# Kernel tuning notes

Measured on AMD Instinct MI355X. Metric: run time of the kernel, lower is better.

Reference implementation:

```python
import jax, jax.numpy as jnp
import numpy as np

G, N, H = 64, 512, 64          # graphs, nodes/graph, hidden
NT = G * N                     # total nodes
DEG = 32
ET = NT * DEG                  # total edges
KP = int(np.ceil(0.7 * N))     # TopKPooling keep per graph (359)
NP2 = G * KP                   # nodes after pooling
F_IN, NC, NA = 128, 2, 6
seg = jax.ops.segment_sum


def graph_norm(h, batch, num_g, w, b, ms, eps=1e-5):
    cnt = seg(jnp.ones((h.shape[0], 1), h.dtype), batch, num_segments=num_g)
    mean = seg(h, batch, num_segments=num_g) / cnt
    hc = h - ms * mean[batch]
    var = seg(hc * hc, batch, num_segments=num_g) / cnt
    return w * hc / jnp.sqrt(var[batch] + eps) + b


def sage(h, src, tgt, valid, Ws, Wn, b, n_nodes):
    # PyG SAGEConv (mean aggr): out_i = x_i@Ws + mean_{j->i} x_j @ Wn + b
    msg = h[src] * valid[:, None]
    agg = seg(msg, tgt, num_segments=n_nodes)
    deg = seg(valid, tgt, num_segments=n_nodes)
    return h @ Ws + (agg / jnp.maximum(deg, 1.0)[:, None]) @ Wn + b


def setup_inputs() -> dict:
    key = jax.random.key(0)
    ks = jax.random.split(key, 20)
    offs = (jnp.arange(G) * N)[:, None]
    src = (jax.random.randint(ks[0], (G, N * DEG), 0, N) + offs).reshape(-1)
    tgt = (jax.random.randint(ks[1], (G, N * DEG), 0, N) + offs).reshape(-1)
    edge_index = jnp.stack([src, tgt])  # within-graph edges

    def lin(k, fi, fo):
        return jax.random.normal(k, (fi, fo), jnp.float32) / np.sqrt(fi)

    return {
        "x": jax.random.normal(ks[2], (NT, F_IN), jnp.float32),
        "edge_index": edge_index,
        "edge_attr": jax.random.uniform(ks[3], (ET,), jnp.float32),
        "coords": jax.random.normal(ks[4], (NT, 3), jnp.float32),
        "anatomical_class": jax.random.randint(ks[5], (NT,), 0, NA),
        "Bk_table": jax.random.normal(ks[6], (NA, H * H), jnp.float32) * 0.05,
        "pos_W": lin(ks[7], 3, H), "pos_b": jnp.zeros((H,), jnp.float32),
        "W1_self": lin(ks[8], F_IN, H), "W1_neigh": lin(ks[9], F_IN, H),
        "b1": jnp.zeros((H,), jnp.float32),
        "gn1_w": jnp.ones((H,), jnp.float32), "gn1_b": jnp.zeros((H,), jnp.float32),
        "gn1_ms": jnp.ones((H,), jnp.float32),
        "pool_p": jax.random.normal(ks[10], (H,), jnp.float32),
        "W2_self": lin(ks[11], H, H), "W2_neigh": lin(ks[12], H, H),
        "b2": jnp.zeros((H,), jnp.float32),
        "gn2_w": jnp.ones((H,), jnp.float32), "gn2_b": jnp.zeros((H,), jnp.float32),
        "gn2_ms": jnp.ones((H,), jnp.float32),
        "lin1_W": lin(ks[13], 3 * H, H), "lin1_b": jnp.zeros((H,), jnp.float32),
        "lin2_W": lin(ks[14], H, NC), "lin2_b": jnp.zeros((NC,), jnp.float32),
    }


def reference(x, edge_index, edge_attr, coords, anatomical_class, Bk_table,
              pos_W, pos_b, W1_self, W1_neigh, b1, gn1_w, gn1_b, gn1_ms,
              pool_p, W2_self, W2_neigh, b2, gn2_w, gn2_b, gn2_ms,
              lin1_W, lin1_b, lin2_W, lin2_b):
    row, col = edge_index[0], edge_index[1]
    batch = jnp.repeat(jnp.arange(G), N)
    # ---- stage 1: anatomical propagation kernel ----
    e = coords @ pos_W + pos_b                                 # [NT, H]
    Ae = seg(edge_attr[:, None] * e[col], row, num_segments=NT)  # SpMM adj @ e
    Bk = Bk_table[anatomical_class].reshape(NT, H, H)
    delta = jnp.einsum('nd,nhd->nh', Ae, Bk)                   # bmm(Ae, Bk^T)
    ones_e = jnp.ones((ET,), x.dtype)
    h = sage(x, row, col, ones_e, W1_self, W1_neigh, b1, NT)
    h = jax.nn.elu(graph_norm(h, batch, G, gn1_w, gn1_b, gn1_ms))
    h = h + delta
    h = jnp.einsum('nij,nj->ni', Bk + delta[:, :, None], h)    # propagate_message
    # ---- TopK pooling (equal-sized graphs) ----
    score = (h @ pool_p) / jnp.linalg.norm(pool_p)
    vals, idx = jax.lax.top_k(score.reshape(G, N), KP)
    perm = (idx + (jnp.arange(G) * N)[:, None]).reshape(-1)    # [NP2]
    h = h[perm] * jnp.tanh(vals).reshape(-1)[:, None]
    batch2 = jnp.repeat(jnp.arange(G), KP)
    node_map = jnp.full((NT,), -1, jnp.int32).at[perm].set(jnp.arange(NP2, dtype=jnp.int32))
    s2, t2 = node_map[row], node_map[col]
    valid = ((s2 >= 0) & (t2 >= 0)).astype(h.dtype)            # masked edge filter
    s2 = jnp.where(s2 >= 0, s2, 0)
    t2 = jnp.where(t2 >= 0, t2, 0)
    # ---- stage 2 ----
    e2 = coords[perm] @ pos_W + pos_b
    Bk2 = Bk_table[anatomical_class[perm]].reshape(NP2, H, H)
    Ae2 = seg(valid[:, None] * e2[t2], s2, num_segments=NP2)   # edge_attr = ones
    delta2 = jnp.einsum('nd,nhd->nh', Ae2, Bk2)
    h = h + delta2
    h = jnp.einsum('nij,nj->ni', Bk2 + delta2[:, :, None], h)
    h = sage(h, s2, t2, valid, W2_self, W2_neigh, b2, NP2)
    h = jax.nn.elu(graph_norm(h, batch2, G, gn2_w, gn2_b, gn2_ms))
    # ---- readout ----
    cnt = seg(jnp.ones((NP2, 1), h.dtype), batch2, num_segments=G)
    hsum = seg(h, batch2, num_segments=G)
    g = jnp.concatenate([hsum / cnt,
                         jax.ops.segment_max(h, batch2, num_segments=G),
                         hsum], axis=1)
    g = jax.nn.relu(g @ lin1_W + lin1_b)
    return jax.nn.log_softmax(g @ lin2_W + lin2_b, axis=1)
```

## Files before the change

### kernel.cpp

```cpp
#include <hip/hip_runtime.h>
#include <math.h>

#define G_    64
#define N_    512
#define H_    64
#define NT_   32768
#define ET_   1048576
#define EPG_  16384
#define KP_   359
#define NP2_  22976
#define FIN_  128
#define ESL_  2048
#define BPB_  (EPG_/ESL_)

__global__ __launch_bounds__(256)
void k_histprep(const int* __restrict__ row, const int* __restrict__ col,
                int* __restrict__ histR8, int* __restrict__ histC8,
                const float* __restrict__ Bk, const float* __restrict__ posW,
                const float* __restrict__ posb,
                float* __restrict__ BkT, float* __restrict__ PT) {
    int b = blockIdx.x, t = threadIdx.x;
    if (b < G_ * BPB_) {
        __shared__ int hr[N_], hc[N_];
        int g = b >> 3, s = b & (BPB_ - 1);
        for (int i = t; i < N_; i += 256) { hr[i] = 0; hc[i] = 0; }
        __syncthreads();
        int ebase = g * EPG_ + s * ESL_;
        for (int i = t; i < ESL_; i += 256) {
            atomicAdd(&hr[row[ebase + i] & (N_ - 1)], 1);
            atomicAdd(&hc[col[ebase + i] & (N_ - 1)], 1);
        }
        __syncthreads();
        int sbase = (g * BPB_ + s) * N_;
        for (int i = t; i < N_; i += 256) {
            histR8[sbase + i] = hr[i];
            histC8[sbase + i] = hc[i];
        }
    } else if (b < G_ * BPB_ + 96) {
        int idx = (b - G_ * BPB_) * 256 + t;
        int c = idx >> 12, r = idx & 4095;
        int h = r >> 6, d = r & 63;
        BkT[c * 4096 + d * 64 + h] = Bk[c * 4096 + h * 64 + d];
    } else {
        int c = b - (G_ * BPB_ + 96);
        int i = t >> 6, h = t & 63;
        const float* B = Bk + c * 4096 + h * 64;
        float acc = 0.f;
        for (int d = 0; d < 64; d++) {
            float vd = (i < 3) ? posW[i*64 + d] : posb[d];
            acc += B[d] * vd;
        }
        PT[c*256 + i*64 + h] = acc;
    }
}

__global__ __launch_bounds__(256)
void k_scan(const int* __restrict__ histR8, const int* __restrict__ histC8,
            int* __restrict__ rowptr, int* __restrict__ colptr,
            float* __restrict__ deg, int* __restrict__ nmap) {
    __shared__ int hr[N_], hc[N_];
    int g = blockIdx.x, t = threadIdx.x;
    int nbase = g * N_;
    for (int i = t; i < N_; i += 256) {
        int sr = 0, sc = 0;
        #pragma unroll
        for (int s = 0; s < BPB_; s++) {
            sr += histR8[(g * BPB_ + s) * N_ + i];
            sc += histC8[(g * BPB_ + s) * N_ + i];
        }
        hr[i] = sr; hc[i] = sc;
        deg[nbase + i] = (float)sc;
        nmap[nbase + i] = -1;
    }
    __syncthreads();
    int wave = t >> 6, lane = t & 63;
    if (wave < 2) {
        int* h = wave ? hc : hr;
        int base8 = lane * 8;
        int loc[8];
        int tot = 0;
        #pragma unroll
        for (int i = 0; i < 8; i++) { int v = h[base8 + i]; loc[i] = tot; tot += v; }
        int pref = tot;
        for (int off = 1; off < 64; off <<= 1) {
            int u = __shfl_up(pref, off);
            if (lane >= off) pref += u;
        }
        pref -= tot;
        #pragma unroll
        for (int i = 0; i < 8; i++) h[base8 + i] = pref + loc[i];
    }
    __syncthreads();
    int ebase = g * EPG_;
    for (int i = t; i < N_; i += 256) {
        rowptr[nbase + i] = ebase + hr[i];
        colptr[nbase + i] = ebase + hc[i];
    }
    if (g == 0 && t == 0) { rowptr[NT_] = ET_; colptr[NT_] = ET_; }
}

__global__ __launch_bounds__(1024)
void k_scat(const int* __restrict__ row, const int* __restrict__ col,
            const float* __restrict__ ea,
            const int* __restrict__ rowptr, const int* __restrict__ colptr,
            int2* __restrict__ rowcsr, int* __restrict__ colcsr) {
    __shared__ int curR[128], curC[128];
    int g = blockIdx.x >> 2, q = blockIdx.x & 3;
    int t = threadIdx.x;
    int lo = q * 128;
    int nbase = g * N_ + lo;
    if (t < 128) { curR[t] = rowptr[nbase + t]; curC[t] = colptr[nbase + t]; }
    __syncthreads();
    int ebase = g * EPG_;
    for (int i = t; i < EPG_; i += 1024) {
        int rg = row[ebase + i];
        int cg = col[ebase + i];
        int rl = (rg & (N_ - 1)) - lo;
        if ((unsigned)rl < 128u) {
            int pr = atomicAdd(&curR[rl], 1);
            rowcsr[pr] = make_int2(cg, __float_as_int(ea[ebase + i]));
        }
        int cl = (cg & (N_ - 1)) - lo;
        if ((unsigned)cl < 128u) {
            int pc = atomicAdd(&curC[cl], 1);
            colcsr[pc] = rg;
        }
    }
}

__global__ __launch_bounds__(256)
void k_gemm_dual(const float* __restrict__ in, int K,
                 const float* __restrict__ Wa, const float* __restrict__ Wb,
                 const float* __restrict__ bias,
                 float* __restrict__ outA, float* __restrict__ outB) {
    __shared__ float inT[32 * FIN_];
    int row0 = blockIdx.x * 32;
    int t = threadIdx.x;
    for (int idx = t; idx < 32 * K; idx += 256) inT[idx] = in[row0 * K + idx];
    __syncthreads();
    int c = t & 63, rb = t >> 6;
    const float* ip = inT + (rb * 8) * K;
    float aA[8] = {0,0,0,0,0,0,0,0};
    float aB[8] = {0,0,0,0,0,0,0,0};
    for (int k = 0; k < K; k += 4) {
        float wa0 = Wa[(k+0)*64 + c], wa1 = Wa[(k+1)*64 + c];
        float wa2 = Wa[(k+2)*64 + c], wa3 = Wa[(k+3)*64 + c];
        float wb0 = Wb[(k+0)*64 + c], wb1 = Wb[(k+1)*64 + c];
        float wb2 = Wb[(k+2)*64 + c], wb3 = Wb[(k+3)*64 + c];
        #pragma unroll
        for (int r = 0; r < 8; r++) {
            float4 xv = *(const float4*)&ip[r*K + k];
            aA[r] += xv.x*wa0; aB[r] += xv.x*wb0;
            aA[r] += xv.y*wa1; aB[r] += xv.y*wb1;
            aA[r] += xv.z*wa2; aB[r] += xv.z*wb2;
            aA[r] += xv.w*wa3; aB[r] += xv.w*wb3;
        }
    }
    float bv = bias[c];
    #pragma unroll
    for (int r = 0; r < 8; r++) {
        int node = row0 + rb*8 + r;
        outA[node*64 + c] = aA[r];
        outB[node*64 + c] = aB[r] + bv;
    }
}

__global__ __launch_bounds__(256)
void k_edge1f(const int* __restrict__ rowptr, const int2* __restrict__ rcsr,
              const int* __restrict__ colptr, const int* __restrict__ ccsr,
              const float* __restrict__ coords, const float* __restrict__ y,
              float4* __restrict__ nsum, float* __restrict__ agg) {
    int node = blockIdx.x * 4 + (threadIdx.x >> 6);
    int lane = threadIdx.x & 63;
    int rs = rowptr[node], re = rowptr[node + 1];
    float sx = 0.f, sy = 0.f, sz = 0.f, sw = 0.f;
    for (int k = rs + lane; k < re; k += 64) {
        int2 ent = rcsr[k];
        int c = ent.x;
        float w = __int_as_float(ent.y);
        sx += w * coords[c*3+0];
        sy += w * coords[c*3+1];
        sz += w * coords[c*3+2];
        sw += w;
    }
    #pragma unroll
    for (int off = 32; off; off >>= 1) {
        sx += __shfl_xor(sx, off); sy += __shfl_xor(sy, off);
        sz += __shfl_xor(sz, off); sw += __shfl_xor(sw, off);
    }
    if (lane == 0) nsum[node] = make_float4(sx, sy, sz, sw);
    int cs = colptr[node], ce = colptr[node + 1];
    float acc = 0.f;
    #pragma unroll 8
    for (int k = cs; k < ce; k++) {
        int r = ccsr[k];
        acc += y[r*64 + lane];
    }
// ... 41 lines not shown
    #pragma unroll
    for (int i = 0; i < 8; i++) {
        s1 += partial[(g*8 + i)*128 + lane];
        s2 += partial[(g*8 + i)*128 + 64 + lane];
    }
    float m  = s1 / (float)N_, q = s2 / (float)N_, msv = ms[lane];
    float var = q - msv * m * m * (2.f - msv);
    float mval = msv * m;
    float istd = rsqrtf(var + 1e-5f);
    float4 s4 = nsum[node];
    int c = cls[node];
    const float* P = PT + c * 256;
    float d = s4.x*P[lane] + s4.y*P[64+lane] + s4.z*P[128+lane] + s4.w*P[192+lane];
    float v = hself[node*64 + lane] + agg[node*64 + lane] / fmaxf(deg[node], 1.f);
    v = w[lane] * (v - mval) * istd + b[lane];
    v = v > 0.f ? v : expm1f(v);
    v += d;
    hT[t] = v;
    __syncthreads();
    float ssum = v;
    #pragma unroll
    for (int off = 32; off; off >>= 1) ssum += __shfl_xor(ssum, off);
    const float* B  = BkT + c * 4096;
    const float* hv = hT + (t & ~63);
    float acc = 0.f;
    #pragma unroll 8
    for (int j = 0; j < 64; j++) acc += B[j*64 + lane] * hv[j];
    out[node*64 + lane] = acc + d * ssum;
}

__global__ __launch_bounds__(512)
void k_topk(const float* __restrict__ hp, const float* __restrict__ p,
            const int* __restrict__ cls, const int* __restrict__ ccsr,
            int* __restrict__ perm, float* __restrict__ tanhv,
            int* __restrict__ node_map, int* __restrict__ class2,
            int* __restrict__ ccsr2) {
    __shared__ float key[N_];
    __shared__ int   idxS[N_];
    __shared__ int   lmap[N_];
    __shared__ float pS[64];
    __shared__ float nrm;
    int g = blockIdx.x, t = threadIdx.x;
    lmap[t] = -1;
    if (t < 64) pS[t] = p[t];
    __syncthreads();
    if (t == 0) {
        float s = 0.f;
        for (int i = 0; i < 64; i++) s += pS[i] * pS[i];
        nrm = sqrtf(s);
    }
    __syncthreads();
    {
        float acc = 0.f;
        const float* hv = hp + (size_t)(g*N_ + t) * 64;
        for (int cdx = 0; cdx < 64; cdx++) acc += hv[cdx] * pS[cdx];
        key[t]  = acc / nrm;
        idxS[t] = t;
    }
    __syncthreads();
    for (int k = 2; k <= N_; k <<= 1) {
        for (int j = k >> 1; j > 0; j >>= 1) {
            int i = t, ixj = i ^ j;
            if (ixj > i) {
                float ki = key[i], kj = key[ixj];
                int   ii = idxS[i], ij = idxS[ixj];
                bool before = (ki > kj) || (ki == kj && ii < ij);
                bool dir = ((i & k) == 0);
                if (dir ? !before : before) {
                    key[i] = kj; key[ixj] = ki;
                    idxS[i] = ij; idxS[ixj] = ii;
                }
            }
            __syncthreads();
        }
    }
    if (t < KP_) {
        int orig  = idxS[t];
        int gnode = g * N_ + orig;
        int pj    = g * KP_ + t;
        perm[pj]     = gnode;
        tanhv[pj]    = tanhf(key[t]);
        node_map[gnode] = pj;
        class2[pj]   = cls[gnode];
        lmap[orig]   = pj;
    }
    __syncthreads();
    int ebase = g * EPG_;
    for (int k = t; k < EPG_; k += 512) {
        int mm = lmap[ccsr[ebase + k] & (N_ - 1)];
        ccsr2[ebase + k] = (mm >= 0) ? mm : NP2_;
    }
}

__global__ __launch_bounds__(256)
void k_s2prop(const int* __restrict__ rowptr, const int2* __restrict__ rcsr,
              const int* __restrict__ colptr, const int* __restrict__ ccsr,
              const int* __restrict__ perm, const int* __restrict__ nmap,
              const float* __restrict__ coords,
              const float* __restrict__ hp, const float* __restrict__ tanhv,
              const int* __restrict__ cls2,
              const float* __restrict__ PT, const float* __restrict__ BkT,
              float* __restrict__ out, float* __restrict__ deg2,
              float* __restrict__ y2zero) {
    __shared__ float hT[256];
    int t = threadIdx.x;
    int j = blockIdx.x * 4 + (t >> 6);
    int lane = t & 63;
    if (blockIdx.x == 0 && t < 64) y2zero[t] = 0.f;
    int orig = perm[j];
    int rs = rowptr[orig], re = rowptr[orig + 1];
    float sx = 0.f, sy = 0.f, sz = 0.f, sw = 0.f;
    for (int k = rs + lane; k < re; k += 64) {
        int c = rcsr[k].x;
        if (nmap[c] >= 0) {
            sx += coords[c*3+0]; sy += coords[c*3+1]; sz += coords[c*3+2];
            sw += 1.f;
        }
    }
    int cs = colptr[orig], ce = colptr[orig + 1];
    float dg = 0.f;
    for (int k = cs + lane; k < ce; k += 64) {
        if (nmap[ccsr[k]] >= 0) dg += 1.f;
    }
    #pragma unroll
    for (int off = 32; off; off >>= 1) {
        sx += __shfl_xor(sx, off); sy += __shfl_xor(sy, off);
        sz += __shfl_xor(sz, off); sw += __shfl_xor(sw, off);
        dg += __shfl_xor(dg, off);
    }
    if (lane == 0) deg2[j] = dg;
    int c = cls2[j];
    const float* P = PT + c * 256;
    float d = sx*P[lane] + sy*P[64+lane] + sz*P[128+lane] + sw*P[192+lane];
    float v = hp[orig*64 + lane] * tanhv[j] + d;
    hT[t] = v;
    __syncthreads();
    float ssum = v;
    #pragma unroll
    for (int off = 32; off; off >>= 1) ssum += __shfl_xor(ssum, off);
    const float* B  = BkT + c * 4096;
    const float* hv = hT + (t & ~63);
    float acc = 0.f;
    #pragma unroll 8
    for (int jj = 0; jj < 64; jj++) acc += B[jj*64 + lane] * hv[jj];
    out[j*64 + lane] = acc + d * ssum;
}

__global__ __launch_bounds__(256)
void k_gagg2(const int* __restrict__ colptr, const int* __restrict__ ccsr2,
             const int* __restrict__ perm, const float* __restrict__ y2,
             float* __restrict__ agg2) {
    int j = blockIdx.x * 4 + (threadIdx.x >> 6);
    int lane = threadIdx.x & 63;
    int orig = perm[j];
    int start = colptr[orig], end = colptr[orig + 1];
    float acc = 0.f;
    #pragma unroll 8
    for (int k = start; k < end; k++) {
        int r = ccsr2[k];
        acc += y2[r*64 + lane];
    }
    agg2[j*64 + lane] = acc;
}
// ... 38 lines not shown

__global__ void k_rfin(const float* __restrict__ part, int CH,
                       const float* __restrict__ l1W, const float* __restrict__ l1b,
                       const float* __restrict__ l2W, const float* __restrict__ l2b,
                       float* __restrict__ out) {
    __shared__ float gv[192], rS[64];
    int g = blockIdx.x, t = threadIdx.x;
    float s = 0.f, m = -1e30f;
    for (int i = 0; i < CH; i++) {
        s += part[(g*CH + i)*128 + t];
        m = fmaxf(m, part[(g*CH + i)*128 + 64 + t]);
    }
    gv[t] = s / (float)KP_;
    gv[64 + t] = m;
    gv[128 + t] = s;
    __syncthreads();
    float acc = l1b[t];
    for (int k = 0; k < 192; k++) acc += gv[k] * l1W[k*64 + t];
    rS[t] = fmaxf(acc, 0.f);
    __syncthreads();
    if (t == 0) {
        float l0 = l2b[0], l1v = l2b[1];
        for (int hh = 0; hh < 64; hh++) { l0 += rS[hh]*l2W[hh*2+0]; l1v += rS[hh]*l2W[hh*2+1]; }
        float mx  = fmaxf(l0, l1v);
        float lse = mx + logf(expf(l0 - mx) + expf(l1v - mx));
        out[g*2 + 0] = l0  - lse;
        out[g*2 + 1] = l1v - lse;
    }
}

extern "C" void kernel_launch(void* const* d_in, const int* in_sizes, int n_in,
                              void* d_out, int out_size, void* d_ws, size_t ws_size,
                              hipStream_t stream) {
    const float* x      = (const float*)d_in[0];
    const int*   eidx   = (const int*)  d_in[1];
    const float* eattr  = (const float*)d_in[2];
    const float* coords = (const float*)d_in[3];
    const int*   acls   = (const int*)  d_in[4];
    const float* BkTab  = (const float*)d_in[5];
    const float* posW   = (const float*)d_in[6];
    const float* posb   = (const float*)d_in[7];
    const float* W1s    = (const float*)d_in[8];
    const float* W1n    = (const float*)d_in[9];
    const float* b1     = (const float*)d_in[10];
    const float* gn1w   = (const float*)d_in[11];
    const float* gn1b   = (const float*)d_in[12];
    const float* gn1ms  = (const float*)d_in[13];
    const float* poolp  = (const float*)d_in[14];
    const float* W2s    = (const float*)d_in[15];
    const float* W2n    = (const float*)d_in[16];
    const float* b2     = (const float*)d_in[17];
    const float* gn2w   = (const float*)d_in[18];
    const float* gn2b   = (const float*)d_in[19];
    const float* gn2ms  = (const float*)d_in[20];
    const float* l1W    = (const float*)d_in[21];
    const float* l1b    = (const float*)d_in[22];
    const float* l2W    = (const float*)d_in[23];
    const float* l2b    = (const float*)d_in[24];

    const int* row  = eidx;
    const int* colp = eidx + ET_;

    float* W = (float*)d_ws;
    const size_t NTH = (size_t)NT_ * 64;
    float* b0    = W;
    float* b1buf = W + 1*NTH;
    float* b2buf = W + 2*NTH;
    float* b3buf = W + 3*NTH;
    float* p = W + 4*NTH;
    int2*  rowcsr = (int2*)p;        p += 2*(size_t)ET_;
    int*   colcsr = (int*)p;         p += ET_;
    int*   ccsr2  = (int*)p;         p += ET_;
    int*   rowptr = (int*)p;         p += NT_ + 8;
    int*   colptr = (int*)p;         p += NT_ + 8;
    int*   histR8 = (int*)p;         p += NT_ * BPB_ / 1;
    int*   histC8 = (int*)p;         p += NT_ * BPB_ / 1;
    float* deg    = p;               p += NT_;
    float* deg2   = p;               p += NP2_;
    float* tanhv  = p;               p += NP2_;
    int*   perm   = (int*)p;         p += NP2_;
    int*   nmap   = (int*)p;         p += NT_;
    int*   cls2   = (int*)p;         p += NP2_;
    float* BkT    = p;               p += 6 * 4096;
    float* PT     = p;               p += 6 * 256;
    float* statsP = p;               p += (size_t)G_ * 8 * 128;
    float* readP  = p;               p += (size_t)G_ * 6 * 128;
    float4* nsum  = (float4*)b3buf;

    k_histprep <<<G_*BPB_ + 102, 256, 0, stream>>>(row, colp, histR8, histC8,
                                                   BkTab, posW, posb, BkT, PT);
    k_scan     <<<G_,      256,  0, stream>>>(histR8, histC8, rowptr, colptr, deg, nmap);
    k_scat     <<<G_*4,    1024, 0, stream>>>(row, colp, eattr, rowptr, colptr,
                                              rowcsr, colcsr);

    k_gemm_dual<<<NT_/32,  256, 0, stream>>>(x, FIN_, W1n, W1s, b1,
                                             b0 , b1buf );
    k_edge1f   <<<NT_/4,   256, 0, stream>>>(rowptr, rowcsr, colptr, colcsr,
                                             coords, b0 , nsum, b2buf );
    k_gnstat   <<<G_*8,    256, 0, stream>>>(b1buf , b2buf , deg,
                                             statsP, N_, 8, 64);
    k_gnprop   <<<NT_/4,   256, 0, stream>>>(b1buf , b2buf , deg,
                                             statsP, gn1ms, gn1w, gn1b,
                                             nsum, acls, PT, BkT,
                                             b1buf );
    k_topk     <<<G_,      512, 0, stream>>>(b1buf , poolp, acls, colcsr,
                                             perm, tanhv, nmap, cls2, ccsr2);

    k_s2prop   <<<NP2_/4,  256, 0, stream>>>(rowptr, rowcsr, colptr, colcsr,
                                             perm, nmap, coords,
                                             b1buf , tanhv, cls2, PT, BkT,
                                             b2buf , deg2,
                                             b0 + (size_t)NP2_ * 64 );
    k_gemm_dual<<<NP2_/32, 256, 0, stream>>>(b2buf , 64, W2n, W2s, b2,
                                             b0 , b3buf );
    k_gagg2    <<<NP2_/4,  256, 0, stream>>>(colptr, ccsr2, perm, b0 ,
                                             b1buf );
    k_gnstat   <<<G_*6,    256, 0, stream>>>(b3buf , b1buf , deg2,
                                             statsP, KP_, 6, 60);
    k_gnrd     <<<G_*6,    256, 0, stream>>>(b3buf , b1buf , deg2,
                                             statsP, gn2ms, gn2w, gn2b, readP);
    k_rfin     <<<G_,      64,  0, stream>>>(readP, 6, l1W, l1b, l2W, l2b,
                                             (float*)d_out);
}
```

Baseline: 335.2 us.

## Fuse all stages into one cooperative persistent kernel with grid syncs

Replaces the chain of about fourteen separate kernel launches with a single cooperative persistent kernel. Each stage loops over its work units, and grid.sync() separates the stages. The change also moves the deg2 computation into the top-k stage and splits the CSR scatter into 64-node slices. The aim is to remove per-launch overhead and inter-kernel gaps, at the cost of grid-wide barriers, a grid size capped by occupancy, and one register/shared-memory budget shared by every stage.

```diff
diff --git a/kernel.cpp b/kernel.cpp
--- a/kernel.cpp
+++ b/kernel.cpp
@@ -1,141 +1,46 @@
 #include <hip/hip_runtime.h>
+#include <hip/hip_cooperative_groups.h>
 #include <math.h>
+
+namespace cg = cooperative_groups;
 
 #define G_    64
 #define N_    512
-#define H_    64
 #define NT_   32768
 #define ET_   1048576
 #define EPG_  16384
 #define KP_   359
 #define NP2_  22976
 #define FIN_  128
-#define ESL_  2048
-#define BPB_  (EPG_/ESL_)
-
-__global__ __launch_bounds__(256)
-void k_histprep(const int* __restrict__ row, const int* __restrict__ col,
-                int* __restrict__ histR8, int* __restrict__ histC8,
-                const float* __restrict__ Bk, const float* __restrict__ posW,
-                const float* __restrict__ posb,
-                float* __restrict__ BkT, float* __restrict__ PT) {
-    int b = blockIdx.x, t = threadIdx.x;
-    if (b < G_ * BPB_) {
-        __shared__ int hr[N_], hc[N_];
-        int g = b >> 3, s = b & (BPB_ - 1);
-        for (int i = t; i < N_; i += 256) { hr[i] = 0; hc[i] = 0; }
-        __syncthreads();
-        int ebase = g * EPG_ + s * ESL_;
-        for (int i = t; i < ESL_; i += 256) {
-            atomicAdd(&hr[row[ebase + i] & (N_ - 1)], 1);
-            atomicAdd(&hc[col[ebase + i] & (N_ - 1)], 1);
-        }
-        __syncthreads();
-        int sbase = (g * BPB_ + s) * N_;
-        for (int i = t; i < N_; i += 256) {
-            histR8[sbase + i] = hr[i];
-            histC8[sbase + i] = hc[i];
-        }
-    } else if (b < G_ * BPB_ + 96) {
-        int idx = (b - G_ * BPB_) * 256 + t;
-        int c = idx >> 12, r = idx & 4095;
-        int h = r >> 6, d = r & 63;
-        BkT[c * 4096 + d * 64 + h] = Bk[c * 4096 + h * 64 + d];
-    } else {
-        int c = b - (G_ * BPB_ + 96);
-        int i = t >> 6, h = t & 63;
-        const float* B = Bk + c * 4096 + h * 64;
-        float acc = 0.f;
-        for (int d = 0; d < 64; d++) {
-            float vd = (i < 3) ? posW[i*64 + d] : posb[d];
-            acc += B[d] * vd;
-        }
-        PT[c*256 + i*64 + h] = acc;
-    }
-}
-
-__global__ __launch_bounds__(256)
-void k_scan(const int* __restrict__ histR8, const int* __restrict__ histC8,
-            int* __restrict__ rowptr, int* __restrict__ colptr,
-            float* __restrict__ deg, int* __restrict__ nmap) {
-    __shared__ int hr[N_], hc[N_];
-    int g = blockIdx.x, t = threadIdx.x;
-    int nbase = g * N_;
-    for (int i = t; i < N_; i += 256) {
-        int sr = 0, sc = 0;
-        #pragma unroll
-        for (int s = 0; s < BPB_; s++) {
-            sr += histR8[(g * BPB_ + s) * N_ + i];
-            sc += histC8[(g * BPB_ + s) * N_ + i];
-        }
-        hr[i] = sr; hc[i] = sc;
-        deg[nbase + i] = (float)sc;
-        nmap[nbase + i] = -1;
-    }
-    __syncthreads();
-    int wave = t >> 6, lane = t & 63;
-    if (wave < 2) {
-        int* h = wave ? hc : hr;
-        int base8 = lane * 8;
-        int loc[8];
-        int tot = 0;
-        #pragma unroll
-        for (int i = 0; i < 8; i++) { int v = h[base8 + i]; loc[i] = tot; tot += v; }
-        int pref = tot;
-        for (int off = 1; off < 64; off <<= 1) {
-            int u = __shfl_up(pref, off);
-            if (lane >= off) pref += u;
-        }
-        pref -= tot;
-        #pragma unroll
-        for (int i = 0; i < 8; i++) h[base8 + i] = pref + loc[i];
-    }
-    __syncthreads();
-    int ebase = g * EPG_;
-    for (int i = t; i < N_; i += 256) {
-        rowptr[nbase + i] = ebase + hr[i];
-        colptr[nbase + i] = ebase + hc[i];
-    }
-    if (g == 0 && t == 0) { rowptr[NT_] = ET_; colptr[NT_] = ET_; }
-}
-
-__global__ __launch_bounds__(1024)
-void k_scat(const int* __restrict__ row, const int* __restrict__ col,
-            const float* __restrict__ ea,
-            const int* __restrict__ rowptr, const int* __restrict__ colptr,
-            int2* __restrict__ rowcsr, int* __restrict__ colcsr) {
-    __shared__ int curR[128], curC[128];
-    int g = blockIdx.x >> 2, q = blockIdx.x & 3;
-    int t = threadIdx.x;
-    int lo = q * 128;
-    int nbase = g * N_ + lo;
-    if (t < 128) { curR[t] = rowptr[nbase + t]; curC[t] = colptr[nbase + t]; }
-    __syncthreads();
-    int ebase = g * EPG_;
-    for (int i = t; i < EPG_; i += 1024) {
-        int rg = row[ebase + i];
-        int cg = col[ebase + i];
-        int rl = (rg & (N_ - 1)) - lo;
-        if ((unsigned)rl < 128u) {
-            int pr = atomicAdd(&curR[rl], 1);
-            rowcsr[pr] = make_int2(cg, __float_as_int(ea[ebase + i]));
-        }
-        int cl = (cg & (N_ - 1)) - lo;
-        if ((unsigned)cl < 128u) {
-            int pc = atomicAdd(&curC[cl], 1);
-            colcsr[pc] = rg;
-        }
-    }
-}
-
-__global__ __launch_bounds__(256)
-void k_gemm_dual(const float* __restrict__ in, int K,
-                 const float* __restrict__ Wa, const float* __restrict__ Wb,
-                 const float* __restrict__ bias,
-                 float* __restrict__ outA, float* __restrict__ outB) {
-    __shared__ float inT[32 * FIN_];
-    int row0 = blockIdx.x * 32;
-    int t = threadIdx.x;
+
+struct Params {
+    const int* row; const int* col; const float* ea;
+    const float* x; const float* coords; const int* acls;
+    const float* Bk; const float* posW; const float* posb;
+    const float* W1s; const float* W1n; const float* b1;
+    const float* gn1w; const float* gn1b; const float* gn1ms;
+    const float* poolp;
+    const float* W2s; const float* W2n; const float* b2;
+    const float* gn2w; const float* gn2b; const float* gn2ms;
+    const float* l1W; const float* l1b; const float* l2W; const float* l2b;
+    float* y; float* hself; float* agg; float* aux;
+    int2* rowcsr; int* colcsr; int* ccsr2;
+    int* rowptr; int* colptr;
+    int* histR8; int* histC8;
+    float* deg; float* deg2; float* tanhv;
+    int* perm; int* nmap; int* cls2;
+    float* BkT; float* PT;
+    float* statsP; float* readP;
+    float* out;
+};
+
+__device__ __forceinline__
+void gemm_unit(int unit, const float* __restrict__ in, int K,
+               const float* __restrict__ Wa, const float* __restrict__ Wb,
+               const float* __restrict__ bias,
+               float* __restrict__ outA, float* __restrict__ outB,
+               float* inT, int t) {
+    int row0 = unit * 32;
     for (int idx = t; idx < 32 * K; idx += 256) inT[idx] = in[row0 * K + idx];
     __syncthreads();
     int c = t & 63, rb = t >> 6;
@@ -163,6 +68,564 @@
         outA[node*64 + c] = aA[r];
         outB[node*64 + c] = aB[r] + bv;
     }
+    __syncthreads();
+}
+
+__global__ __launch_bounds__(256)
+void k_mega(Params P) {
+    cg::grid_group grid = cg::this_grid();
+    __shared__ float smemF[4096];
+    int* smemI = (int*)smemF;
+    const int t = threadIdx.x;
+    const int bx = blockIdx.x;
+    const int NBg = gridDim.x;
+
+    for (int b = bx; b < 614; b += NBg) {
+        if (b < 512) {
+            int g = b >> 3, s = b & 7;
+            int* hr = smemI; int* hc = smemI + N_;
+            for (int i = t; i < N_; i += 256) { hr[i] = 0; hc[i] = 0; }
+            __syncthreads();
+            int ebase = g * EPG_ + s * 2048;
+            for (int i = t; i < 2048; i += 256) {
+                atomicAdd(&hr[P.row[ebase + i] & (N_ - 1)], 1);
+                atomicAdd(&hc[P.col[ebase + i] & (N_ - 1)], 1);
+            }
+            __syncthreads();
+            int sbase = b * N_;
+            for (int i = t; i < N_; i += 256) {
+                P.histR8[sbase + i] = hr[i];
+                P.histC8[sbase + i] = hc[i];
+            }
+            __syncthreads();
+        } else if (b < 608) {
+            int idx = (b - 512) * 256 + t;
+            int c = idx >> 12, r = idx & 4095;
+            int h = r >> 6, d = r & 63;
+            P.BkT[c*4096 + d*64 + h] = P.Bk[c*4096 + h*64 + d];
+        } else {
+            int c = b - 608;
+            int i = t >> 6, h = t & 63;
+            const float* B = P.Bk + c*4096 + h*64;
+            float acc = 0.f;
+            for (int d = 0; d < 64; d++) {
+                float vd = (i < 3) ? P.posW[i*64 + d] : P.posb[d];
+                acc += B[d] * vd;
+            }
+            P.PT[c*256 + i*64 + h] = acc;
+        }
+    }
+    grid.sync();
+
+    for (int g = bx; g < G_; g += NBg) {
+        int* hr = smemI; int* hc = smemI + N_;
+        int nbase = g * N_;
+        for (int i = t; i < N_; i += 256) {
+            int sr = 0, sc = 0;
+            #pragma unroll
+            for (int s = 0; s < 8; s++) {
+                sr += P.histR8[(g*8 + s)*N_ + i];
+                sc += P.histC8[(g*8 + s)*N_ + i];
+            }
+            hr[i] = sr; hc[i] = sc;
+            P.deg[nbase + i] = (float)sc;
+            P.nmap[nbase + i] = -1;
+        }
+        __syncthreads();
+        int wave = t >> 6, lane = t & 63;
+        if (wave < 2) {
+            int* h = wave ? hc : hr;
+            int base8 = lane * 8;
+            int loc[8];
+            int tot = 0;
+            #pragma unroll
+            for (int i = 0; i < 8; i++) { int v = h[base8 + i]; loc[i] = tot; tot += v; }
+            int pref = tot;
+            for (int off = 1; off < 64; off <<= 1) {
+                int u = __shfl_up(pref, off);
+                if (lane >= off) pref += u;
+            }
+            pref -= tot;
+            #pragma unroll
+            for (int i = 0; i < 8; i++) h[base8 + i] = pref + loc[i];
+        }
+        __syncthreads();
+        int ebase = g * EPG_;
+        for (int i = t; i < N_; i += 256) {
+            P.rowptr[nbase + i] = ebase + hr[i];
+            P.colptr[nbase + i] = ebase + hc[i];
+        }
+        if (g == 0 && t == 0) { P.rowptr[NT_] = ET_; P.colptr[NT_] = ET_; }
+        __syncthreads();
+    }
+    grid.sync();
+
+    for (int b = bx; b < 512; b += NBg) {
+        int g = b >> 3, q = b & 7;
+        int lo = q * 64;
+        int* curR = smemI; int* curC = smemI + 64;
+        int nbase = g * N_ + lo;
+        if (t < 64) { curR[t] = P.rowptr[nbase + t]; curC[t] = P.colptr[nbase + t]; }
+        __syncthreads();
+        int ebase = g * EPG_;
+        for (int i = t; i < EPG_; i += 256) {
+            int rg = P.row[ebase + i];
+            int cg2 = P.col[ebase + i];
+            int rl = (rg & (N_ - 1)) - lo;
+            if ((unsigned)rl < 64u) {
+                int pr = atomicAdd(&curR[rl], 1);
+                P.rowcsr[pr] = make_int2(cg2, __float_as_int(P.ea[ebase + i]));
+            }
+            int cl = (cg2 & (N_ - 1)) - lo;
+            if ((unsigned)cl < 64u) {
+                int pc = atomicAdd(&curC[cl], 1);
+                P.colcsr[pc] = rg;
+            }
+        }
+        __syncthreads();
+    }
+    grid.sync();
+
+    for (int u = bx; u < NT_/32; u += NBg)
+        gemm_unit(u, P.x, FIN_, P.W1n, P.W1s, P.b1, P.y, P.hself, smemF, t);
+    grid.sync();
+
+    {
+        float4* nsum = (float4*)P.aux;
+        for (int u = bx; u < NT_/4; u += NBg) {
+            int node = u * 4 + (t >> 6);
+            int lane = t & 63;
+            int rs = P.rowptr[node], re = P.rowptr[node + 1];
+            float sx = 0.f, sy = 0.f, sz = 0.f, sw = 0.f;
+            for (int k = rs + lane; k < re; k += 64) {
+                int2 ent = P.rowcsr[k];
+                int c = ent.x;
+                float w = __int_as_float(ent.y);
+                sx += w * P.coords[c*3+0];
+                sy += w * P.coords[c*3+1];
+                sz += w * P.coords[c*3+2];
+                sw += w;
+            }
+            #pragma unroll
+            for (int off = 32; off; off >>= 1) {
+                sx += __shfl_xor(sx, off); sy += __shfl_xor(sy, off);
+                sz += __shfl_xor(sz, off); sw += __shfl_xor(sw, off);
+            }
+            if (lane == 0) nsum[node] = make_float4(sx, sy, sz, sw);
+            int cs = P.colptr[node], ce = P.colptr[node + 1];
+            float acc = 0.f;
+            #pragma unroll 8
+            for (int k = cs; k < ce; k++) {
+                int r = P.colcsr[k];
+                acc += P.y[r*64 + lane];
+            }
+            P.agg[node*64 + lane] = acc;
+        }
+    }
+    grid.sync();
+
+    for (int b = bx; b < G_*8; b += NBg) {
+        float* r1 = smemF; float* r2 = smemF + 256;
+        int g = b >> 3, chunk = b & 7;
+        int c = t & 63, grp = t >> 6;
+        int n0 = chunk * 64;
+        float s1 = 0.f, s2 = 0.f;
+        for (int n = n0 + grp; n < n0 + 64; n += 4) {
+            int node = g * N_ + n;
+            float v = P.hself[node*64 + c] + P.agg[node*64 + c] / fmaxf(P.deg[node], 1.f);
+            s1 += v; s2 += v * v;
+        }
+        r1[t] = s1; r2[t] = s2;
+        __syncthreads();
+        if (grp == 0) {
+            P.statsP[b*128 + c]      = r1[c] + r1[64+c] + r1[128+c] + r1[192+c];
+            P.statsP[b*128 + 64 + c] = r2[c] + r2[64+c] + r2[128+c] + r2[192+c];
+        }
+        __syncthreads();
+    }
+    grid.sync();
+
+    {
+        float4* nsum = (float4*)P.aux;
+        for (int u = bx; u < NT_/4; u += NBg) {
+            float* hT = smemF;
+            int node = u * 4 + (t >> 6);
+            int lane = t & 63;
+            int g = node >> 9;
+            float s1 = 0.f, s2 = 0.f;
+            #pragma unroll
+            for (int i = 0; i < 8; i++) {
+                s1 += P.statsP[(g*8 + i)*128 + lane];
+                s2 += P.statsP[(g*8 + i)*128 + 64 + lane];
+            }
+            float m = s1 / (float)N_, q = s2 / (float)N_, msv = P.gn1ms[lane];
+            float var = q - msv * m * m * (2.f - msv);
+            float mval = msv * m;
+            float istd = rsqrtf(var + 1e-5f);
+            float4 s4 = nsum[node];
+            int c = P.acls[node];
+            const float* Pt = P.PT + c * 256;
+            float d = s4.x*Pt[lane] + s4.y*Pt[64+lane] + s4.z*Pt[128+lane] + s4.w*Pt[192+lane];
+            float v = P.hself[node*64 + lane] + P.agg[node*64 + lane] / fmaxf(P.deg[node], 1.f);
+            v = P.gn1w[lane] * (v - mval) * istd + P.gn1b[lane];
+            v = v > 0.f ? v : expm1f(v);
+            v += d;
+            hT[t] = v;
+            __syncthreads();
+            float ssum = v;
+            #pragma unroll
+            for (int off = 32; off; off >>= 1) ssum += __shfl_xor(ssum, off);
+            const float* B  = P.BkT + c * 4096;
+            const float* hv = hT + (t & ~63);
+            float acc = 0.f;
+            #pragma unroll 8
+            for (int j = 0; j < 64; j++) acc += B[j*64 + lane] * hv[j];
+            P.hself[node*64 + lane] = acc + d * ssum;
+            __syncthreads();
+        }
+    }
+    grid.sync();
+
+    for (int g = bx; g < G_; g += NBg) {
+        float* key = smemF;
+        int* idxS  = smemI + 512;
+        int* lmap  = smemI + 1024;
+        int* ideg  = smemI + 1536;
+        float* pS  = smemF + 1936;
+        if (t < 64) pS[t] = P.poolp[t];
+        lmap[t] = -1; lmap[t + 256] = -1;
+        for (int i = t; i < KP_; i += 256) ideg[i] = 0;
+        __syncthreads();
+        float nrm;
+        {
+            float s = 0.f;
+            for (int i = 0; i < 64; i++) s += pS[i] * pS[i];
+            nrm = sqrtf(s);
+        }
+        for (int n = t; n < N_; n += 256) {
+            float acc = 0.f;
+            const float* hv = P.hself + (size_t)(g*N_ + n) * 64;
+            for (int cdx = 0; cdx < 64; cdx++) acc += hv[cdx] * pS[cdx];
+            key[n]  = acc / nrm;
+            idxS[n] = n;
+        }
+        __syncthreads();
+        for (int k = 2; k <= N_; k <<= 1) {
+            for (int j = k >> 1; j > 0; j >>= 1) {
+                for (int i0 = t; i0 < N_; i0 += 256) {
+                    int i = i0, ixj = i ^ j;
+                    if (ixj > i) {
+                        float ki = key[i], kj = key[ixj];
+                        int   ii = idxS[i], ij = idxS[ixj];
+                        bool before = (ki > kj) || (ki == kj && ii < ij);
+                        bool dir = ((i & k) == 0);
+                        if (dir ? !before : before) {
+                            key[i] = kj; key[ixj] = ki;
+                            idxS[i] = ij; idxS[ixj] = ii;
+                        }
+                    }
+                }
+                __syncthreads();
+            }
+        }
+        for (int n = t; n < KP_; n += 256) {
+            int orig  = idxS[n];
+            int gnode = g * N_ + orig;
+            int pj    = g * KP_ + n;
+            P.perm[pj]  = gnode;
+            P.tanhv[pj] = tanhf(key[n]);
+            P.nmap[gnode] = pj;
+            P.cls2[pj]  = P.acls[gnode];
+            lmap[orig]  = pj;
+        }
+        __syncthreads();
+        int ebase = g * EPG_;
+        for (int k = t; k < EPG_; k += 256) {
+            int mm = lmap[P.colcsr[ebase + k] & (N_ - 1)];
+            P.ccsr2[ebase + k] = (mm >= 0) ? mm : NP2_;
+        }
+        for (int k = t; k < EPG_; k += 256) {
+            int mr = lmap[P.row[ebase + k] & (N_ - 1)];
+            int mc = lmap[P.col[ebase + k] & (N_ - 1)];
+            if (mr >= 0 && mc >= 0) atomicAdd(&ideg[mc - g * KP_], 1);
+        }
+        __syncthreads();
+        for (int i = t; i < KP_; i += 256) P.deg2[g * KP_ + i] = (float)ideg[i];
+        __syncthreads();
+    }
+    grid.sync();
+
+    if (bx == 0 && t < 64) P.y[(size_t)NP2_ * 64 + t] = 0.f;
+    for (int u = bx; u < NP2_/4; u += NBg) {
+        float* hT = smemF;
+        int j = u * 4 + (t >> 6);
+        int lane = t & 63;
+        int orig = P.perm[j];
+        int rs = P.rowptr[orig], re = P.rowptr[orig + 1];
+        float sx = 0.f, sy = 0.f, sz = 0.f, sw = 0.f;
+        for (int k = rs + lane; k < re; k += 64) {
+            int c = P.rowcsr[k].x;
+            if (P.nmap[c] >= 0) {
+                sx += P.coords[c*3+0]; sy += P.coords[c*3+1]; sz += P.coords[c*3+2];
+                sw += 1.f;
+            }
+        }
+        #pragma unroll
+        for (int off = 32; off; off >>= 1) {
+            sx += __shfl_xor(sx, off); sy += __shfl_xor(sy, off);
+            sz += __shfl_xor(sz, off); sw += __shfl_xor(sw, off);
+        }
+        int c = P.cls2[j];
+        const float* Pt = P.PT + c * 256;
+        float d = sx*Pt[lane] + sy*Pt[64+lane] + sz*Pt[128+lane] + sw*Pt[192+lane];
+        float v = P.hself[orig*64 + lane] * P.tanhv[j] + d;
+        hT[t] = v;
+        __syncthreads();
+        float ssum = v;
+        #pragma unroll
+        for (int off = 32; off; off >>= 1) ssum += __shfl_xor(ssum, off);
+        const float* B  = P.BkT + c * 4096;
+        const float* hv = hT + (t & ~63);
+        float acc = 0.f;
+        #pragma unroll 8
+        for (int jj = 0; jj < 64; jj++) acc += B[jj*64 + lane] * hv[jj];
+        P.agg[j*64 + lane] = acc + d * ssum;
+        __syncthreads();
+    }
+    grid.sync();
+
+    for (int u = bx; u < NP2_/32; u += NBg)
+        gemm_unit(u, P.agg, 64, P.W2n, P.W2s, P.b2, P.y, P.aux, smemF, t);
+    grid.sync();
+
+    for (int u = bx; u < NP2_/4; u += NBg) {
+        int j = u * 4 + (t >> 6);
+        int lane = t & 63;
+        int orig = P.perm[j];
+        int start = P.colptr[orig], end = P.colptr[orig + 1];
+        float acc = 0.f;
+        #pragma unroll 8
+        for (int k = start; k < end; k++) {
+            int r = P.ccsr2[k];
+            acc += P.y[r*64 + lane];
+        }
+        P.hself[j*64 + lane] = acc;
+    }
+    grid.sync();
+
+    for (int b = bx; b < G_*6; b += NBg) {
+        float* r1 = smemF; float* r2 = smemF + 256;
+        int g = b / 6, chunk = b % 6;
+        int c = t & 63, grp = t >> 6;
+        int n0 = chunk * 60, nend = min(n0 + 60, KP_);
+        float s1 = 0.f, s2 = 0.f;
+        for (int n = n0 + grp; n < nend; n += 4) {
+            int node = g * KP_ + n;
+            float v = P.aux[node*64 + c] + P.hself[node*64 + c] / fmaxf(P.deg2[node], 1.f);
+            s1 += v; s2 += v * v;
+        }
+        r1[t] = s1; r2[t] = s2;
+        __syncthreads();
+        if (grp == 0) {
+            P.statsP[b*128 + c]      = r1[c] + r1[64+c] + r1[128+c] + r1[192+c];
+            P.statsP[b*128 + 64 + c] = r2[c] + r2[64+c] + r2[128+c] + r2[192+c];
+        }
+        __syncthreads();
+    }
+    grid.sync();
+
+    for (int b = bx; b < G_*6; b += NBg) {
+        float* r1 = smemF; float* r2 = smemF + 256;
+        int g = b / 6, chunk = b % 6;
+        int c = t & 63, grp = t >> 6;
+        float s1 = 0.f, s2 = 0.f;
+        #pragma unroll
+        for (int i = 0; i < 6; i++) {
+            s1 += P.statsP[(g*6 + i)*128 + c];
+            s2 += P.statsP[(g*6 + i)*128 + 64 + c];
+        }
+        float mean = s1 / (float)KP_, q = s2 / (float)KP_, msv = P.gn2ms[c];
+        float var = q - msv * mean * mean * (2.f - msv);
+        float mv = msv * mean;
+        float is = rsqrtf(var + 1e-5f);
+        float wv = P.gn2w[c], bv = P.gn2b[c];
+        int n0 = chunk * 60, nend = min(n0 + 60, KP_);
+        float s = 0.f, m = -1e30f;
+        for (int n = n0 + grp; n < nend; n += 4) {
+            int node = g * KP_ + n;
+            float v = P.aux[node*64 + c] + P.hself[node*64 + c] / fmaxf(P.deg2[node], 1.f);
+            v = wv * (v - mv) * is + bv;
+            v = v > 0.f ? v : expm1f(v);
+            s += v; m = fmaxf(m, v);
+        }
+        r1[t] = s; r2[t] = m;
+        __syncthreads();
+        if (grp == 0) {
+            P.readP[b*128 + c]      = r1[c] + r1[64+c] + r1[128+c] + r1[192+c];
+            P.readP[b*128 + 64 + c] = fmaxf(fmaxf(r2[c], r2[64+c]), fmaxf(r2[128+c], r2[192+c]));
+        }
+        __syncthreads();
+    }
+    grid.sync();
+
+    for (int g = bx; g < G_; g += NBg) {
+        float* gv = smemF;
+        float* rS = smemF + 192;
+        if (t < 64) {
+            float s = 0.f, m = -1e30f;
+            for (int i = 0; i < 6; i++) {
+                s += P.readP[(g*6 + i)*128 + t];
+                m = fmaxf(m, P.readP[(g*6 + i)*128 + 64 + t]);
+            }
+            gv[t] = s / (float)KP_;
+            gv[64 + t] = m;
+            gv[128 + t] = s;
+        }
+        __syncthreads();
+        if (t < 64) {
+            float acc = P.l1b[t];
+            for (int k = 0; k < 192; k++) acc += gv[k] * P.l1W[k*64 + t];
+            rS[t] = fmaxf(acc, 0.f);
+        }
+        __syncthreads();
+        if (t == 0) {
+            float l0 = P.l2b[0], l1v = P.l2b[1];
+            for (int hh = 0; hh < 64; hh++) {
+                l0  += rS[hh] * P.l2W[hh*2+0];
+                l1v += rS[hh] * P.l2W[hh*2+1];
+            }
+            float mx  = fmaxf(l0, l1v);
+            float lse = mx + logf(expf(l0 - mx) + expf(l1v - mx));
+            P.out[g*2 + 0] = l0  - lse;
+            P.out[g*2 + 1] = l1v - lse;
+        }
+        __syncthreads();
+    }
+}
+
+
+__global__ __launch_bounds__(256)
+void k_histprep(const int* __restrict__ row, const int* __restrict__ col,
+                int* __restrict__ histR8, int* __restrict__ histC8,
+                const float* __restrict__ Bk, const float* __restrict__ posW,
+                const float* __restrict__ posb,
+                float* __restrict__ BkT, float* __restrict__ PT) {
+    int b = blockIdx.x, t = threadIdx.x;
+    if (b < 512) {
+        __shared__ int hr[N_], hc[N_];
+        int g = b >> 3, s = b & 7;
+        for (int i = t; i < N_; i += 256) { hr[i] = 0; hc[i] = 0; }
+        __syncthreads();
+        int ebase = g * EPG_ + s * 2048;
+        for (int i = t; i < 2048; i += 256) {
+            atomicAdd(&hr[row[ebase + i] & (N_ - 1)], 1);
+            atomicAdd(&hc[col[ebase + i] & (N_ - 1)], 1);
+        }
+        __syncthreads();
+        int sbase = b * N_;
+        for (int i = t; i < N_; i += 256) {
+            histR8[sbase + i] = hr[i];
+            histC8[sbase + i] = hc[i];
+        }
+    } else if (b < 608) {
+        int idx = (b - 512) * 256 + t;
+        int c = idx >> 12, r = idx & 4095;
+        int h = r >> 6, d = r & 63;
+        BkT[c*4096 + d*64 + h] = Bk[c*4096 + h*64 + d];
+    } else {
+        int c = b - 608;
+        int i = t >> 6, h = t & 63;
+        const float* B = Bk + c*4096 + h*64;
+        float acc = 0.f;
+        for (int d = 0; d < 64; d++) {
+            float vd = (i < 3) ? posW[i*64 + d] : posb[d];
+            acc += B[d] * vd;
+        }
+        PT[c*256 + i*64 + h] = acc;
+    }
+}
+
+__global__ __launch_bounds__(256)
+void k_scan(const int* __restrict__ histR8, const int* __restrict__ histC8,
+            int* __restrict__ rowptr, int* __restrict__ colptr,
+            float* __restrict__ deg, int* __restrict__ nmap) {
+    __shared__ int hr[N_], hc[N_];
+    int g = blockIdx.x, t = threadIdx.x;
+    int nbase = g * N_;
+    for (int i = t; i < N_; i += 256) {
+        int sr = 0, sc = 0;
+        #pragma unroll
+        for (int s = 0; s < 8; s++) {
+            sr += histR8[(g*8 + s)*N_ + i];
+            sc += histC8[(g*8 + s)*N_ + i];
+        }
+        hr[i] = sr; hc[i] = sc;
+        deg[nbase + i] = (float)sc;
+        nmap[nbase + i] = -1;
+    }
+    __syncthreads();
+    int wave = t >> 6, lane = t & 63;
+    if (wave < 2) {
+        int* h = wave ? hc : hr;
+        int base8 = lane * 8;
+        int loc[8];
+        int tot = 0;
+        #pragma unroll
+        for (int i = 0; i < 8; i++) { int v = h[base8 + i]; loc[i] = tot; tot += v; }
+        int pref = tot;
+        for (int off = 1; off < 64; off <<= 1) {
+            int u = __shfl_up(pref, off);
+            if (lane >= off) pref += u;
+        }
+        pref -= tot;
+        #pragma unroll
+        for (int i = 0; i < 8; i++) h[base8 + i] = pref + loc[i];
+    }
+    __syncthreads();
+    int ebase = g * EPG_;
+    for (int i = t; i < N_; i += 256) {
+        rowptr[nbase + i] = ebase + hr[i];
+        colptr[nbase + i] = ebase + hc[i];
+    }
+    if (g == 0 && t == 0) { rowptr[NT_] = ET_; colptr[NT_] = ET_; }
+}
+
+__global__ __launch_bounds__(1024)
+void k_scat(const int* __restrict__ row, const int* __restrict__ col,
+            const float* __restrict__ ea,
+            const int* __restrict__ rowptr, const int* __restrict__ colptr,
+            int2* __restrict__ rowcsr, int* __restrict__ colcsr) {
+    __shared__ int curR[128], curC[128];
+    int g = blockIdx.x >> 2, q = blockIdx.x & 3;
+    int t = threadIdx.x;
+    int lo = q * 128;
+    int nbase = g * N_ + lo;
+    if (t < 128) { curR[t] = rowptr[nbase + t]; curC[t] = colptr[nbase + t]; }
+    __syncthreads();
+    int ebase = g * EPG_;
+    for (int i = t; i < EPG_; i += 1024) {
+        int rg = row[ebase + i];
+        int cg = col[ebase + i];
+        int rl = (rg & (N_ - 1)) - lo;
+        if ((unsigned)rl < 128u) {
+            int pr = atomicAdd(&curR[rl], 1);
+            rowcsr[pr] = make_int2(cg, __float_as_int(ea[ebase + i]));
+        }
+        int cl = (cg & (N_ - 1)) - lo;
+        if ((unsigned)cl < 128u) {
+            int pc = atomicAdd(&curC[cl], 1);
+            colcsr[pc] = rg;
+        }
+    }
+}
+
+__global__ __launch_bounds__(256)
+void k_gemm_dual(const float* __restrict__ in, int K,
+                 const float* __restrict__ Wa, const float* __restrict__ Wb,
+                 const float* __restrict__ bias,
+                 float* __restrict__ outA, float* __restrict__ outB) {
+    __shared__ float inT[32 * FIN_];
+    gemm_unit(blockIdx.x, in, K, Wa, Wb, bias, outA, outB, inT, threadIdx.x);
 }
 
 __global__ __launch_bounds__(256)
@@ -270,17 +733,20 @@
 __global__ __launch_bounds__(512)
 void k_topk(const float* __restrict__ hp, const float* __restrict__ p,
             const int* __restrict__ cls, const int* __restrict__ ccsr,
+            const int* __restrict__ row, const int* __restrict__ col,
             int* __restrict__ perm, float* __restrict__ tanhv,
             int* __restrict__ node_map, int* __restrict__ class2,
-            int* __restrict__ ccsr2) {
+            int* __restrict__ ccsr2, float* __restrict__ deg2) {
     __shared__ float key[N_];
     __shared__ int   idxS[N_];
     __shared__ int   lmap[N_];
+    __shared__ int   ideg[KP_];
     __shared__ float pS[64];
     __shared__ float nrm;
     int g = blockIdx.x, t = threadIdx.x;
     lmap[t] = -1;
     if (t < 64) pS[t] = p[t];
+    for (int i = t; i < KP_; i += 512) ideg[i] = 0;
     __syncthreads();
     if (t == 0) {
         float s = 0.f;
@@ -328,18 +794,23 @@
         int mm = lmap[ccsr[ebase + k] & (N_ - 1)];
         ccsr2[ebase + k] = (mm >= 0) ? mm : NP2_;
     }
+    for (int k = t; k < EPG_; k += 512) {
+        int mr = lmap[row[ebase + k] & (N_ - 1)];
+        int mc = lmap[col[ebase + k] & (N_ - 1)];
+        if (mr >= 0 && mc >= 0) atomicAdd(&ideg[mc - g * KP_], 1);
+    }
+    __syncthreads();
+    for (int i = t; i < KP_; i += 512) deg2[g * KP_ + i] = (float)ideg[i];
 }
 
 __global__ __launch_bounds__(256)
 void k_s2prop(const int* __restrict__ rowptr, const int2* __restrict__ rcsr,
-              const int* __restrict__ colptr, const int* __restrict__ ccsr,
               const int* __restrict__ perm, const int* __restrict__ nmap,
               const float* __restrict__ coords,
               const float* __restrict__ hp, const float* __restrict__ tanhv,
               const int* __restrict__ cls2,
               const float* __restrict__ PT, const float* __restrict__ BkT,
-              float* __restrict__ out, float* __restrict__ deg2,
-              float* __restrict__ y2zero) {
+              float* __restrict__ out, float* __restrict__ y2zero) {
     __shared__ float hT[256];
     int t = threadIdx.x;
     int j = blockIdx.x * 4 + (t >> 6);
@@ -355,18 +826,11 @@
             sw += 1.f;
         }
     }
-    int cs = colptr[orig], ce = colptr[orig + 1];
-    float dg = 0.f;
-    for (int k = cs + lane; k < ce; k += 64) {
-        if (nmap[ccsr[k]] >= 0) dg += 1.f;
-    }
     #pragma unroll
     for (int off = 32; off; off >>= 1) {
         sx += __shfl_xor(sx, off); sy += __shfl_xor(sy, off);
         sz += __shfl_xor(sz, off); sw += __shfl_xor(sw, off);
-        dg += __shfl_xor(dg, off);
-    }
-    if (lane == 0) deg2[j] = dg;
+    }
     int c = cls2[j];
     const float* P = PT + c * 256;
     float d = sx*P[lane] + sy*P[64+lane] + sz*P[128+lane] + sw*P[192+lane];
@@ -471,35 +935,6 @@
 extern "C" void kernel_launch(void* const* d_in, const int* in_sizes, int n_in,
                               void* d_out, int out_size, void* d_ws, size_t ws_size,
                               hipStream_t stream) {
-    const float* x      = (const float*)d_in[0];
-    const int*   eidx   = (const int*)  d_in[1];
-    const float* eattr  = (const float*)d_in[2];
-    const float* coords = (const float*)d_in[3];
-    const int*   acls   = (const int*)  d_in[4];
-    const float* BkTab  = (const float*)d_in[5];
-    const float* posW   = (const float*)d_in[6];
-    const float* posb   = (const float*)d_in[7];
-    const float* W1s    = (const float*)d_in[8];
-    const float* W1n    = (const float*)d_in[9];
-    const float* b1     = (const float*)d_in[10];
-    const float* gn1w   = (const float*)d_in[11];
-    const float* gn1b   = (const float*)d_in[12];
-    const float* gn1ms  = (const float*)d_in[13];
-    const float* poolp  = (const float*)d_in[14];
-    const float* W2s    = (const float*)d_in[15];
-    const float* W2n    = (const float*)d_in[16];
-    const float* b2     = (const float*)d_in[17];
-    const float* gn2w   = (const float*)d_in[18];
-    const float* gn2b   = (const float*)d_in[19];
-    const float* gn2ms  = (const float*)d_in[20];
-    const float* l1W    = (const float*)d_in[21];
-    const float* l1b    = (const float*)d_in[22];
-    const float* l2W    = (const float*)d_in[23];
-    const float* l2b    = (const float*)d_in[24];
-
-    const int* row  = eidx;
-    const int* colp = eidx + ET_;
-
     float* W = (float*)d_ws;
     const size_t NTH = (size_t)NT_ * 64;
     float* b0    = W;
@@ -512,8 +947,8 @@
     int*   ccsr2  = (int*)p;         p += ET_;
     int*   rowptr = (int*)p;         p += NT_ + 8;
     int*   colptr = (int*)p;         p += NT_ + 8;
-    int*   histR8 = (int*)p;         p += NT_ * BPB_ / 1;
-    int*   histC8 = (int*)p;         p += NT_ * BPB_ / 1;
+    int*   histR8 = (int*)p;         p += NT_ * 8;
+    int*   histC8 = (int*)p;         p += NT_ * 8;
     float* deg    = p;               p += NT_;
     float* deg2   = p;               p += NP2_;
     float* tanhv  = p;               p += NP2_;
@@ -524,40 +959,90 @@
     float* PT     = p;               p += 6 * 256;
     float* statsP = p;               p += (size_t)G_ * 8 * 128;
     float* readP  = p;               p += (size_t)G_ * 6 * 128;
-    float4* nsum  = (float4*)b3buf;
-
-    k_histprep <<<G_*BPB_ + 102, 256, 0, stream>>>(row, colp, histR8, histC8,
-                                                   BkTab, posW, posb, BkT, PT);
-    k_scan     <<<G_,      256,  0, stream>>>(histR8, histC8, rowptr, colptr, deg, nmap);
-    k_scat     <<<G_*4,    1024, 0, stream>>>(row, colp, eattr, rowptr, colptr,
-                                              rowcsr, colcsr);
-
-    k_gemm_dual<<<NT_/32,  256, 0, stream>>>(x, FIN_, W1n, W1s, b1,
-                                             b0 , b1buf );
-    k_edge1f   <<<NT_/4,   256, 0, stream>>>(rowptr, rowcsr, colptr, colcsr,
-                                             coords, b0 , nsum, b2buf );
-    k_gnstat   <<<G_*8,    256, 0, stream>>>(b1buf , b2buf , deg,
-                                             statsP, N_, 8, 64);
-    k_gnprop   <<<NT_/4,   256, 0, stream>>>(b1buf , b2buf , deg,
-                                             statsP, gn1ms, gn1w, gn1b,
-                                             nsum, acls, PT, BkT,
-                                             b1buf );
-    k_topk     <<<G_,      512, 0, stream>>>(b1buf , poolp, acls, colcsr,
-                                             perm, tanhv, nmap, cls2, ccsr2);
-
-    k_s2prop   <<<NP2_/4,  256, 0, stream>>>(rowptr, rowcsr, colptr, colcsr,
-                                             perm, nmap, coords,
-                                             b1buf , tanhv, cls2, PT, BkT,
-                                             b2buf , deg2,
-                                             b0 + (size_t)NP2_ * 64 );
-    k_gemm_dual<<<NP2_/32, 256, 0, stream>>>(b2buf , 64, W2n, W2s, b2,
-                                             b0 , b3buf );
-    k_gagg2    <<<NP2_/4,  256, 0, stream>>>(colptr, ccsr2, perm, b0 ,
-                                             b1buf );
-    k_gnstat   <<<G_*6,    256, 0, stream>>>(b3buf , b1buf , deg2,
-                                             statsP, KP_, 6, 60);
-    k_gnrd     <<<G_*6,    256, 0, stream>>>(b3buf , b1buf , deg2,
-                                             statsP, gn2ms, gn2w, gn2b, readP);
-    k_rfin     <<<G_,      64,  0, stream>>>(readP, 6, l1W, l1b, l2W, l2b,
-                                             (float*)d_out);
-}
+
+    Params P;
+    P.row    = (const int*)d_in[1];
+    P.col    = (const int*)d_in[1] + ET_;
+    P.ea     = (const float*)d_in[2];
+    P.x      = (const float*)d_in[0];
+    P.coords = (const float*)d_in[3];
+    P.acls   = (const int*)d_in[4];
+    P.Bk     = (const float*)d_in[5];
+    P.posW   = (const float*)d_in[6];
+    P.posb   = (const float*)d_in[7];
+    P.W1s    = (const float*)d_in[8];
+    P.W1n    = (const float*)d_in[9];
+    P.b1     = (const float*)d_in[10];
+    P.gn1w   = (const float*)d_in[11];
+    P.gn1b   = (const float*)d_in[12];
+    P.gn1ms  = (const float*)d_in[13];
+    P.poolp  = (const float*)d_in[14];
+    P.W2s    = (const float*)d_in[15];
+    P.W2n    = (const float*)d_in[16];
+    P.b2     = (const float*)d_in[17];
+    P.gn2w   = (const float*)d_in[18];
+    P.gn2b   = (const float*)d_in[19];
+    P.gn2ms  = (const float*)d_in[20];
+    P.l1W    = (const float*)d_in[21];
+    P.l1b    = (const float*)d_in[22];
+    P.l2W    = (const float*)d_in[23];
+    P.l2b    = (const float*)d_in[24];
+    P.y = b0; P.hself = b1buf; P.agg = b2buf; P.aux = b3buf;
+    P.rowcsr = rowcsr; P.colcsr = colcsr; P.ccsr2 = ccsr2;
+    P.rowptr = rowptr; P.colptr = colptr;
+    P.histR8 = histR8; P.histC8 = histC8;
+    P.deg = deg; P.deg2 = deg2; P.tanhv = tanhv;
+    P.perm = perm; P.nmap = nmap; P.cls2 = cls2;
+    P.BkT = BkT; P.PT = PT; P.statsP = statsP; P.readP = readP;
+    P.out = (float*)d_out;
+
+    int blocksPerCU = 0;
+    hipError_t qerr = hipOccupancyMaxActiveBlocksPerMultiprocessor(
+        &blocksPerCU, (const void*)k_mega, 256, 0);
+    int dev = 0, ncu = 0;
+    hipGetDevice(&dev);
+    hipDeviceGetAttribute(&ncu, hipDeviceAttributeMultiprocessorCount, dev);
+    long grid = (long)blocksPerCU * (long)ncu;
+    if (grid > 1024) grid = 1024;
+
+    hipError_t lerr = hipErrorUnknown;
+    if (qerr == hipSuccess && grid >= 64) {
+        void* args[] = { &P };
+        lerr = hipLaunchCooperativeKernel((const void*)k_mega, dim3((int)grid),
+                                          dim3(256), args, 0, stream);
+    }
+    if (lerr != hipSuccess) {
+        const int* row  = P.row;
+        const int* colp = P.col;
+        float4* nsum = (float4*)b3buf;
+        k_histprep <<<614,     256,  0, stream>>>(row, colp, histR8, histC8,
+                                                  P.Bk, P.posW, P.posb, BkT, PT);
+        k_scan     <<<G_,      256,  0, stream>>>(histR8, histC8, rowptr, colptr,
+                                                  deg, nmap);
+        k_scat     <<<G_*4,    1024, 0, stream>>>(row, colp, P.ea, rowptr, colptr,
+                                                  rowcsr, colcsr);
+        k_gemm_dual<<<NT_/32,  256, 0, stream>>>(P.x, FIN_, P.W1n, P.W1s, P.b1,
+                                                 b0, b1buf);
+        k_edge1f   <<<NT_/4,   256, 0, stream>>>(rowptr, rowcsr, colptr, colcsr,
+                                                 P.coords, b0, nsum, b2buf);
+        k_gnstat   <<<G_*8,    256, 0, stream>>>(b1buf, b2buf, deg, statsP, N_, 8, 64);
+        k_gnprop   <<<NT_/4,   256, 0, stream>>>(b1buf, b2buf, deg, statsP, P.gn1ms,
+                                                 P.gn1w, P.gn1b, nsum, P.acls,
+                                                 PT, BkT, b1buf);
+        k_topk     <<<G_,      512, 0, stream>>>(b1buf, P.poolp, P.acls, colcsr,
+                                                 row, colp, perm, tanhv, nmap,
+                                                 cls2, ccsr2, deg2);
+        k_s2prop   <<<NP2_/4,  256, 0, stream>>>(rowptr, rowcsr, perm, nmap,
+                                                 P.coords, b1buf, tanhv, cls2,
+                                                 PT, BkT, b2buf,
+                                                 b0 + (size_t)NP2_ * 64);
+        k_gemm_dual<<<NP2_/32, 256, 0, stream>>>(b2buf, 64, P.W2n, P.W2s, P.b2,
+                                                 b0, b3buf);
+        k_gagg2    <<<NP2_/4,  256, 0, stream>>>(colptr, ccsr2, perm, b0, b1buf);
+        k_gnstat   <<<G_*6,    256, 0, stream>>>(b3buf, b1buf, deg2, statsP, KP_, 6, 60);
+        k_gnrd     <<<G_*6,    256, 0, stream>>>(b3buf, b1buf, deg2, statsP,
+                                                 P.gn2ms, P.gn2w, P.gn2b, readP);
+        k_rfin     <<<G_,      64,  0, stream>>>(readP, 6, P.l1W, P.l1b,
+                                                 P.l2W, P.l2b, (float*)d_out);
+    }
+}
```

New measurement: 1.314 ms. 292% more time.
